# Kernel tuning notes

Measured on AMD Instinct MI355X. Metric: run time of the kernel, lower is better.

The kernel has to match this reference:

```python
import jax, jax.numpy as jnp
import numpy as np

FREQ_DIM = 64
BLOCK_DIM = 64
N = 256          # lattice sites
CH = 6           # channel_num -> block diagonals at offsets -1, 0, +1
S = 2 * 16 + CH - 2   # seq_num = 36
BS = 4           # block_size (kron of two 2x2 matrices)
HID = 128
EPS = 1e-5
B = 32

_e = np.eye(2)
_sx = np.array([[0., 1.], [1., 0.]])
_siy = np.array([[0., 1.], [-1., 0.]])
_sz = np.array([[1., 0.], [0., -1.]])
_p = [_e, _sx, _siy, _sz]
KRONS = jnp.asarray(np.stack([np.kron(_p[a], _p[b]) for a in range(4) for b in range(4)]).astype(np.float32))  # (16,4,4)
Z1 = KRONS[12]  # kron(sigma_z, I) used for interaction blocks ('z1')


def _bn(h, g, b):
    # BatchNorm1d in training mode: biased batch statistics over axis 0
    mu = h.mean(axis=0)
    v = h.var(axis=0)
    return g * (h - mu) / jnp.sqrt(v + EPS) + b


def _mlp(x, Win, bin_, Wmid, bmid, Wout, bout, gamma, beta):
    # depth-4 MLP: Lin+ReLU, then (BN,Lin,ReLU) x2, then BN,Lin,ReLU
    h = jax.nn.relu(x @ Win + bin_)
    for i in range(Wmid.shape[0]):
        h = jax.nn.relu(_bn(h, gamma[i], beta[i]) @ Wmid[i] + bmid[i])
    return jax.nn.relu(_bn(h, gamma[-1], beta[-1]) @ Wout + bout)


def _lstm(xs, h0, c0, Wih, Whh, bih, bhh):
    # xs: (B, T, S); torch gate order i, f, g, o
    def step(carry, x_t):
        h, c = carry
        gates = x_t @ Wih.T + h @ Whh.T + (bih + bhh)
        i, f, g, o = jnp.split(gates, 4, axis=-1)
        c = jax.nn.sigmoid(f) * c + jax.nn.sigmoid(i) * jnp.tanh(g)
        h = jax.nn.sigmoid(o) * jnp.tanh(c)
        return (h, c), h
    _, hs = jax.lax.scan(step, (h0, c0), jnp.swapaxes(xs, 0, 1))
    return jnp.swapaxes(hs, 0, 1)


def setup_inputs() -> dict:
    key = jax.random.key(0)
    ks = iter(jax.random.split(key, 48))
    def w(shape, s=0.05):
        return jax.random.normal(next(ks), shape, dtype=jnp.float32) * s
    d = {
        'x': w((B, FREQ_DIM + BLOCK_DIM), 1.0),
        'fd_Win': w((FREQ_DIM, HID)), 'fd_bin': w((HID,)),
        'fd_Wmid': w((2, HID, HID)), 'fd_bmid': w((2, HID)),
        'fd_Wout': w((HID, S)), 'fd_bout': w((S,)),
        'fd_gamma': jnp.ones((3, HID), jnp.float32), 'fd_beta': jnp.zeros((3, HID), jnp.float32),
        'bd_Win': w((BLOCK_DIM, HID)), 'bd_bin': w((HID,)),
        'bd_Wmid': w((2, HID, HID)), 'bd_bmid': w((2, HID)),
        'bd_Wout': w((HID, S)), 'bd_bout': w((S,)),
        'bd_gamma': jnp.ones((3, HID), jnp.float32), 'bd_beta': jnp.zeros((3, HID), jnp.float32),
        'sc_Win': w((S, 1, HID)), 'sc_bin': w((S, HID)),
        'sc_Wmid': w((S, 2, HID, HID)), 'sc_bmid': w((S, 2, HID)),
        'sc_Wout': w((S, HID, N)), 'sc_bout': w((S, N)),
        'sc_gamma': jnp.ones((S, 3, HID), jnp.float32), 'sc_beta': jnp.zeros((S, 3, HID), jnp.float32),
        'lstm_Wih': w((4 * S, S)), 'lstm_Whh': w((4 * S, S)),
        'lstm_bih': w((4 * S,)), 'lstm_bhh': w((4 * S,)),
        'mix_W': w((S, 2 * S)), 'mix_b': w((S,)),
    }
    return d


def reference(x, fd_Win, fd_bin, fd_Wmid, fd_bmid, fd_Wout, fd_bout, fd_gamma, fd_beta,
              bd_Win, bd_bin, bd_Wmid, bd_bmid, bd_Wout, bd_bout, bd_gamma, bd_beta,
              sc_Win, sc_bin, sc_Wmid, sc_bmid, sc_Wout, sc_bout, sc_gamma, sc_beta,
              lstm_Wih, lstm_Whh, lstm_bih, lstm_bhh, mix_W, mix_b):
    Bsz = x.shape[0]
    block = _mlp(x[:, FREQ_DIM:], bd_Win, bd_bin, bd_Wmid, bd_bmid, bd_Wout, bd_bout, bd_gamma, bd_beta)  # (B,S)
    freq = _mlp(x[:, :FREQ_DIM], fd_Win, fd_bin, fd_Wmid, fd_bmid, fd_Wout, fd_bout, fd_gamma, fd_beta)   # (B,S)
    # S independent scalar->N MLPs, batched with vmap over the stacked params
    sc = jax.vmap(_mlp)(freq.T[:, :, None], sc_Win, sc_bin, sc_Wmid, sc_bmid,
                        sc_Wout, sc_bout, sc_gamma, sc_beta)  # (S,B,N)
    freq_seq = jnp.cos(sc).transpose(1, 2, 0)   # (B,N,S)
    seq = _lstm(freq_seq, block, jnp.zeros_like(block), lstm_Wih, lstm_Whh, lstm_bih, lstm_bhh)  # (B,N,S)
    block_seq = jnp.concatenate([jnp.broadcast_to(block[:, :, None], (Bsz, S, N)),
                                 jnp.swapaxes(seq, 1, 2)], axis=1)  # (B,2S,N)
    # 1x1 Conv2d == channel mixing matmul
    mixed = jnp.einsum('bcn,oc->bon', block_seq, mix_W) + mix_b[None, :, None]  # (B,S,N)
    inter = mixed[:, :CH - 2]                          # (B,CH-2,N)
    onsite = mixed[:, CH - 2:].reshape(Bsz, 2, 16, N)  # (B,2,16,N)
    H_int = jnp.einsum('bcn,ij->bcnij', inter, Z1)         # (B,CH-2,N,4,4)
    H_os = jnp.einsum('bgkn,kij->bgnij', onsite, KRONS)    # (B,2,N,4,4) summed over 16 pairs
    half = (CH - 2) // 2
    strips = jnp.concatenate([H_int[:, :half], H_os, H_int[:, half:]], axis=1)  # (B,CH,N,4,4)
    strips = strips.reshape(Bsz, CH // 2, 2, N, BS, BS)
    # banded block assembly: strip i lives on block-diagonal offset i - (CH//2)//2
    grid = jnp.zeros((Bsz, 2, N, N, BS, BS), dtype=x.dtype)
    for i in range(CH // 2):
        o = i - (CH // 2) // 2
        rows = jnp.arange(N - abs(o)) + max(0, -o)
        cols = rows + o
        grid = grid.at[:, :, rows, cols].set(strips[:, i][:, :, rows])
    matrix = grid.transpose(0, 1, 2, 4, 3, 5).reshape(Bsz, 2, N * BS, N * BS)
    return matrix
```

## Files before the change

### kernel.cpp

```cpp
#include <hip/hip_runtime.h>
#include <math.h>

#define EPSF 1e-5f
typedef __attribute__((ext_vector_type(2))) float f32x2;
typedef __attribute__((ext_vector_type(4))) float f32x4;

__device__ __forceinline__ float pauliv(int p, int r, int c) {
    switch (p) {
        case 0: return (r == c) ? 1.f : 0.f;
        case 1: return (r != c) ? 1.f : 0.f;
        case 2: return (r == 0 && c == 1) ? 1.f : ((r == 1 && c == 0) ? -1.f : 0.f);
        default: return (r == c) ? ((r == 0) ? 1.f : -1.f) : 0.f;
    }
}

__device__ void mlp64_body(const float* __restrict__ xin,
                           const float* __restrict__ Win,
                           const float* __restrict__ bin_,
                           const float* __restrict__ Wmid,
                           const float* __restrict__ bmid,
                           const float* __restrict__ Wout,
                           const float* __restrict__ bout,
                           const float* __restrict__ gamma,
                           const float* __restrict__ beta,
                           float* __restrict__ out)
{
    __shared__ float sX[2048];
    __shared__ float sA[4096];
    __shared__ float sB[4096];
    __shared__ float sMu[128], sRs[128];
    int tid = threadIdx.x;

    for (int idx = tid; idx < 2048; idx += 1024) {
        int b = idx >> 6, c = idx & 63;
        sX[idx] = xin[b * 128 + c];
    }
    __syncthreads();

    for (int idx = tid; idx < 4096; idx += 1024) {
        int b = idx >> 7, j = idx & 127;
        float acc = bin_[j];
        for (int c = 0; c < 64; ++c) acc = fmaf(sX[b * 64 + c], Win[c * 128 + j], acc);
        sA[idx] = fmaxf(acc, 0.f);
    }
    __syncthreads();

    float* cur = sA;
    float* nxt = sB;
    for (int l = 0; l < 3; ++l) {
        if (tid < 128) {
            float s = 0.f, s2 = 0.f;
            for (int b = 0; b < 32; ++b) {
                float v = cur[b * 128 + tid];
                s += v; s2 += v * v;
            }
            float mu = s * (1.f / 32.f);
            float var = s2 * (1.f / 32.f) - mu * mu;
            sMu[tid] = mu;
            sRs[tid] = rsqrtf(var + EPSF);
        }
        __syncthreads();
        for (int idx = tid; idx < 4096; idx += 1024) {
            int j = idx & 127;
            cur[idx] = gamma[l * 128 + j] * (cur[idx] - sMu[j]) * sRs[j] + beta[l * 128 + j];
        }
        __syncthreads();
        if (l < 2) {
            for (int idx = tid; idx < 4096; idx += 1024) {
                int b = idx >> 7, j = idx & 127;
                float acc = bmid[l * 128 + j];
                for (int c = 0; c < 128; ++c)
                    acc = fmaf(cur[b * 128 + c], Wmid[(l * 128 + c) * 128 + j], acc);
                nxt[idx] = fmaxf(acc, 0.f);
            }
            __syncthreads();
            float* t = cur; cur = nxt; nxt = t;
        } else {
            for (int idx = tid; idx < 1152; idx += 1024) {
                int b = idx / 36, j = idx - b * 36;
                float acc = bout[j];
                for (int c = 0; c < 128; ++c)
                    acc = fmaf(cur[b * 128 + c], Wout[c * 36 + j], acc);
                out[idx] = fmaxf(acc, 0.f);
            }
        }
    }
}

__global__ __launch_bounds__(1024) void k_mlp2(
    const float* __restrict__ x,
    const float* fdWin, const float* fdbin, const float* fdWmid, const float* fdbmid,
    const float* fdWout, const float* fdbout, const float* fdg, const float* fdbt,
    const float* bdWin, const float* bdbin, const float* bdWmid, const float* bdbmid,
    const float* bdWout, const float* bdbout, const float* bdg, const float* bdbt,
    float* freq, float* blk)
{
    if (blockIdx.x == 0)
        mlp64_body(x + 64, bdWin, bdbin, bdWmid, bdbmid, bdWout, bdbout, bdg, bdbt, blk);
    else
        mlp64_body(x, fdWin, fdbin, fdWmid, fdbmid, fdWout, fdbout, fdg, fdbt, freq);
}

__global__ __launch_bounds__(512) void k_sc1(
    const float* __restrict__ freq,
    const float* __restrict__ Win,
    const float* __restrict__ bin_,
    const float* __restrict__ Wmid,
    const float* __restrict__ bmid,
    const float* __restrict__ gamma,
    const float* __restrict__ beta,
    float* __restrict__ actW)
{
    int s = blockIdx.x, tid = threadIdx.x;
    __shared__ float sA[4096];
    __shared__ float sB[4096];
    __shared__ float sMu[128], sRs[128];
    const float* Wm = Wmid + (size_t)s * 2 * 128 * 128;
    const float* gm = gamma + s * 3 * 128;
    const float* bt = beta + s * 3 * 128;

    for (int idx = tid; idx < 4096; idx += 512) {
        int b = idx >> 7, j = idx & 127;
        float acc = fmaf(freq[b * 36 + s], Win[s * 128 + j], bin_[s * 128 + j]);
        sA[idx] = fmaxf(acc, 0.f);
    }
    __syncthreads();

    float* cur = sA;
    float* nxt = sB;
    for (int l = 0; l < 3; ++l) {
        if (tid < 128) {
            float sm = 0.f, s2 = 0.f;
            for (int b = 0; b < 32; ++b) {
                float v = cur[b * 128 + tid];
                sm += v; s2 += v * v;
            }
            float mu = sm * (1.f / 32.f);
            float var = s2 * (1.f / 32.f) - mu * mu;
            sMu[tid] = mu;
            sRs[tid] = rsqrtf(var + EPSF);
        }
        __syncthreads();
        for (int idx = tid; idx < 4096; idx += 512) {
            int j = idx & 127;
            cur[idx] = gm[l * 128 + j] * (cur[idx] - sMu[j]) * sRs[j] + bt[l * 128 + j];
        }
        __syncthreads();
        if (l < 2) {
            int jj = tid & 127, bb = tid >> 7;
            float acc[8];
            #pragma unroll
            for (int k = 0; k < 8; ++k) acc[k] = bmid[(s * 2 + l) * 128 + jj];
            for (int c = 0; c < 128; ++c) {
                float w = Wm[(l * 128 + c) * 128 + jj];
                #pragma unroll
                for (int k = 0; k < 8; ++k)
                    acc[k] = fmaf(cur[(bb + 4 * k) * 128 + c], w, acc[k]);
            }
            __syncthreads();
            #pragma unroll
            for (int k = 0; k < 8; ++k) nxt[(bb + 4 * k) * 128 + jj] = fmaxf(acc[k], 0.f);
            __syncthreads();
            float* t = cur; cur = nxt; nxt = t;
        } else {
            for (int idx = tid; idx < 4096; idx += 512)
                actW[(size_t)s * 4096 + idx] = cur[idx];
        }
    }
}

__global__ __launch_bounds__(512) void k_sc2(
    const float* __restrict__ actW,
    const float* __restrict__ Wout,
    const float* __restrict__ bout,
    float* __restrict__ fseq2)
{
    int bidx = blockIdx.x;
    int s = bidx >> 2, q = bidx & 3;
    int tid = threadIdx.x;
    __shared__ float sAct[4096];
    for (int idx = tid; idx < 4096; idx += 512)
        sAct[idx] = actW[(size_t)s * 4096 + idx];
    __syncthreads();

    int nn = (tid & 63) + q * 64;
    int bb = tid >> 6;
    const float* Wo = Wout + (size_t)s * 128 * 256;
    float acc[4];
    #pragma unroll
    for (int k = 0; k < 4; ++k) acc[k] = bout[s * 256 + nn];
    #pragma unroll 4
    for (int c = 0; c < 128; ++c) {
        float w = Wo[c * 256 + nn];
        #pragma unroll
        for (int k = 0; k < 4; ++k)
            acc[k] = fmaf(sAct[(bb + 8 * k) * 128 + c], w, acc[k]);
    }
    #pragma unroll
    for (int k = 0; k < 4; ++k) {
        float v = fmaxf(acc[k], 0.f);
        fseq2[((size_t)s * 32 + bb + 8 * k) * 256 + nn] = __cosf(v);
    }
}

__global__ __launch_bounds__(512) void k_xg(
    const float* __restrict__ fseq2, const float* __restrict__ Wih,
    const float* __restrict__ bih, const float* __restrict__ bhh,
    float* __restrict__ Xg)
{
    int t = blockIdx.x, tid = threadIdx.x;
    __shared__ float sF[1152];
    __shared__ float sWt[36 * 144];
    for (int idx = tid; idx < 1152; idx += 512) {
        int s = idx >> 5, b = idx & 31;
        sF[b * 36 + s] = fseq2[(size_t)idx * 256 + t];
    }
    for (int idx = tid; idx < 5184; idx += 512) {
        int j = idx / 36, s = idx - j * 36;
        sWt[s * 144 + j] = Wih[idx];
    }
    __syncthreads();
    for (int idx = tid; idx < 4608; idx += 512) {
        int b = idx / 144, j = idx - b * 144;
        int g = j / 36, u = j - g * 36;
        float acc = bih[j] + bhh[j];
        #pragma unroll
        for (int s = 0; s < 36; ++s)
            acc = fmaf(sF[b * 36 + s], sWt[s * 144 + j], acc);
        Xg[(((size_t)b * 256 + t) * 36 + u) * 4 + g] = acc;
    }
}

#define PF 8
__global__ __launch_bounds__(64, 1) void k_lstm(
    const float* __restrict__ Xg,
    const float* __restrict__ blk,
    const float* __restrict__ Whh,
    float* __restrict__ hseq2)
{
    int b = blockIdx.x;
    int lane = threadIdx.x;
    int uu = lane < 36 ? lane : 35;
    bool active = lane < 36;

    f32x2 wif[36], wgo[36];
    #pragma unroll
    for (int k = 0; k < 36; ++k) {
        wif[k] = f32x2{Whh[uu * 36 + k], Whh[(36 + uu) * 36 + k]};
        wgo[k] = f32x2{Whh[(72 + uu) * 36 + k], Whh[(108 + uu) * 36 + k]};
    }
    float h = blk[b * 36 + uu];
    float c = 0.f;
    const f32x4* xb = (const f32x4*)(Xg + (size_t)b * 256 * 144);
    float* hout = hseq2 + (size_t)b * 256 * 36;

    f32x4 pipe[PF];
    #pragma unroll
    for (int i = 0; i < PF; ++i) pipe[i] = xb[i * 36 + uu];

    #pragma unroll 8
    for (int t = 0; t < 256; ++t) {
        f32x4 xg4 = pipe[t & (PF - 1)];
        if (t + PF < 256) pipe[t & (PF - 1)] = xb[(t + PF) * 36 + uu];

        f32x2 a0 = f32x2{xg4.x, xg4.y};
        f32x2 b0 = f32x2{xg4.z, xg4.w};
        f32x2 a1 = f32x2{0.f, 0.f};
        f32x2 b1 = f32x2{0.f, 0.f};
        #pragma unroll
        for (int k = 0; k < 36; k += 2) {
            float h0 = __int_as_float(__builtin_amdgcn_readlane(__float_as_int(h), k));
            float h1 = __int_as_float(__builtin_amdgcn_readlane(__float_as_int(h), k + 1));
            a0 = __builtin_elementwise_fma(wif[k], f32x2{h0, h0}, a0);
            b0 = __builtin_elementwise_fma(wgo[k], f32x2{h0, h0}, b0);
            a1 = __builtin_elementwise_fma(wif[k + 1], f32x2{h1, h1}, a1);
            b1 = __builtin_elementwise_fma(wgo[k + 1], f32x2{h1, h1}, b1);
        }
        a0 += a1; b0 += b1;
        float iv = 1.f / (1.f + __expf(-a0.x));
        float fv = 1.f / (1.f + __expf(-a0.y));
        float gv = 1.f - 2.f / (__expf(2.f * b0.x) + 1.f);
        float ov = 1.f / (1.f + __expf(-b0.y));
        c = fmaf(fv, c, iv * gv);
        h = ov * (1.f - 2.f / (__expf(2.f * c) + 1.f));
        if (active) hout[t * 36 + uu] = h;
    }
}

__global__ __launch_bounds__(256) void k_mixed(
    const float* __restrict__ blk, const float* __restrict__ hseq2,
    const float* __restrict__ mixW, const float* __restrict__ mixb,
    float* __restrict__ mixed)
{
    int bq = blockIdx.x;
    int b = bq >> 2, oq = bq & 3;
    int tid = threadIdx.x;
    __shared__ float sH[256 * 37];
    __shared__ float sW[9 * 36];
    __shared__ float sBase[9];
    for (int idx = tid; idx < 9216; idx += 256) {
        int t = idx / 36, u = idx - t * 36;
        sH[t * 37 + u] = hseq2[(size_t)b * 9216 + idx];
    }
    for (int idx = tid; idx < 9 * 36; idx += 256) {
        int o = idx / 36, u = idx - o * 36;
        sW[idx] = mixW[(oq * 9 + o) * 72 + 36 + u];
    }
    if (tid < 9) {
        int o = oq * 9 + tid;
        float acc = mixb[o];
        for (int c = 0; c < 36; ++c) acc = fmaf(mixW[o * 72 + c], blk[b * 36 + c], acc);
        sBase[tid] = acc;
    }
    __syncthreads();
    int n = tid;
    #pragma unroll
    for (int o = 0; o < 9; ++o) {
        float acc = sBase[o];
        #pragma unroll
        for (int u = 0; u < 36; ++u)
            acc = fmaf(sW[o * 36 + u], sH[n * 37 + u], acc);
        mixed[((size_t)b * 36 + oq * 9 + o) * 256 + n] = acc;
    }
}

__global__ __launch_bounds__(256) void k_out(
    const float* __restrict__ mixed, float* __restrict__ out)
{
    int bid = blockIdx.x;
    int bg = bid >> 5, chunk = bid & 31;
    int g = bg & 1, b = bg >> 1;
    float* base = out + (size_t)bg * (1024 * 1024);
    f32x4* rp = (f32x4*)(base + (size_t)chunk * 32 * 1024);
    f32x4 z = f32x4{0.f, 0.f, 0.f, 0.f};
    #pragma unroll
    for (int i = 0; i < 32; ++i)
        rp[i * 256 + threadIdx.x] = z;
    __syncthreads();

    int tid = threadIdx.x;
    if (tid < 8) {
        int n = chunk * 8 + tid;
        const float* mb = mixed + (size_t)b * 36 * 256;
        float vSub = mb[(size_t)g * 256 + n];
        float vSup = mb[(size_t)(2 + g) * 256 + n];
        float ch[16];
        #pragma unroll
        for (int k = 0; k < 16; ++k) ch[k] = mb[(size_t)(4 + 16 * g + k) * 256 + n];
        float d[16];
        #pragma unroll
        for (int e = 0; e < 16; ++e) {
            int r = e >> 2, cc = e & 3;
            float acc = 0.f;
            #pragma unroll
            for (int k = 0; k < 16; ++k) {
                float kv = pauliv(k >> 2, r >> 1, cc >> 1) * pauliv(k & 3, r & 1, cc & 1);
                if (kv == 1.f) acc = acc + ch[k];
                else if (kv == -1.f) acc = acc - ch[k];
            }
            d[e] = acc;
        }
        #pragma unroll
        for (int r = 0; r < 4; ++r)
            *(f32x4*)(base + (size_t)(4 * n + r) * 1024 + 4 * n) =
                f32x4{d[r * 4 + 0], d[r * 4 + 1], d[r * 4 + 2], d[r * 4 + 3]};
        if (n > 0) {
            #pragma unroll
            for (int r = 0; r < 4; ++r)
                base[(size_t)(4 * n + r) * 1024 + 4 * (n - 1) + r] = (r < 2) ? vSub : -vSub;
        }
        if (n < 255) {
            #pragma unroll
            for (int r = 0; r < 4; ++r)
                base[(size_t)(4 * n + r) * 1024 + 4 * (n + 1) + r] = (r < 2) ? vSup : -vSup;
        }
    }
}

extern "C" void kernel_launch(void* const* d_in, const int* in_sizes, int n_in,
                              void* d_out, int out_size, void* d_ws, size_t ws_size,
                              hipStream_t stream) {
    const float* x      = (const float*)d_in[0];
    const float* fdWin  = (const float*)d_in[1];
    const float* fdbin  = (const float*)d_in[2];
    const float* fdWmid = (const float*)d_in[3];
    const float* fdbmid = (const float*)d_in[4];
    const float* fdWout = (const float*)d_in[5];
    const float* fdbout = (const float*)d_in[6];
    const float* fdg    = (const float*)d_in[7];
    const float* fdbt   = (const float*)d_in[8];
    const float* bdWin  = (const float*)d_in[9];
    const float* bdbin  = (const float*)d_in[10];
    const float* bdWmid = (const float*)d_in[11];
    const float* bdbmid = (const float*)d_in[12];
    const float* bdWout = (const float*)d_in[13];
    const float* bdbout = (const float*)d_in[14];
    const float* bdg    = (const float*)d_in[15];
    const float* bdbt   = (const float*)d_in[16];
    const float* scWin  = (const float*)d_in[17];
    const float* scbin  = (const float*)d_in[18];
    const float* scWmid = (const float*)d_in[19];
    const float* scbmid = (const float*)d_in[20];
    const float* scWout = (const float*)d_in[21];
    const float* scbout = (const float*)d_in[22];
    const float* scg    = (const float*)d_in[23];
    const float* scbt   = (const float*)d_in[24];
    const float* Wih    = (const float*)d_in[25];
    const float* Whh    = (const float*)d_in[26];
    const float* bih    = (const float*)d_in[27];
    const float* bhh    = (const float*)d_in[28];
    const float* mixW   = (const float*)d_in[29];
    const float* mixb   = (const float*)d_in[30];

    float* ws    = (float*)d_ws;
    float* freq  = ws;
    float* blk   = ws + 1152;
    float* fseq2 = ws + 2304;
    float* Xg    = ws + 297216;
    float* hseq2 = ws + 1476864;
    float* mixed = ws + 1771776;
    float* actW  = Xg;

    float* out = (float*)d_out;

    k_mlp2<<<2, 1024, 0, stream>>>(x,
        fdWin, fdbin, fdWmid, fdbmid, fdWout, fdbout, fdg, fdbt,
        bdWin, bdbin, bdWmid, bdbmid, bdWout, bdbout, bdg, bdbt,
        freq, blk);
    k_sc1<<<36, 512, 0, stream>>>(freq, scWin, scbin, scWmid, scbmid, scg, scbt, actW);
    k_sc2<<<144, 512, 0, stream>>>(actW, scWout, scbout, fseq2);
    k_xg<<<256, 512, 0, stream>>>(fseq2, Wih, bih, bhh, Xg);
    k_lstm<<<32, 64, 0, stream>>>(Xg, blk, Whh, hseq2);
    k_mixed<<<128, 256, 0, stream>>>(blk, hseq2, mixW, mixb, mixed);
    k_out<<<2048, 256, 0, stream>>>(mixed, out);
}
```

Baseline: 350.9 us.

## Split LSTM gate computation across two wavefronts with LDS exchange

The LSTM recurrence kernel now runs two wavefronts per batch element. Each computes two of the four gates, so the per-lane matvec work and register footprint are halved. The g/o gate activations are passed through shared memory to wave 0, which updates the cell and hidden state and broadcasts h back through LDS. This trades serial FMA latency per timestep for two block-wide barriers per step on the critical recurrence path.

```diff
diff --git a/kernel.cpp b/kernel.cpp
--- a/kernel.cpp
+++ b/kernel.cpp
@@ -4,6 +4,9 @@
 #define EPSF 1e-5f
 typedef __attribute__((ext_vector_type(2))) float f32x2;
 typedef __attribute__((ext_vector_type(4))) float f32x4;
+
+__device__ __forceinline__ float sigf(float x) { return 1.f / (1.f + __expf(-x)); }
+__device__ __forceinline__ float tanhf_fast(float x) { return 1.f - 2.f / (__expf(2.f * x) + 1.f); }
 
 __device__ __forceinline__ float pauliv(int p, int r, int c) {
     switch (p) {
@@ -232,58 +235,71 @@
 }
 
 #define PF 8
-__global__ __launch_bounds__(64, 1) void k_lstm(
+__global__ __launch_bounds__(128) void k_lstm(
     const float* __restrict__ Xg,
     const float* __restrict__ blk,
     const float* __restrict__ Whh,
     float* __restrict__ hseq2)
 {
+    __shared__ f32x2 sGO[40];
+    __shared__ float sH[40];
+
     int b = blockIdx.x;
-    int lane = threadIdx.x;
+    int wid = threadIdx.x >> 6;
+    int lane = threadIdx.x & 63;
     int uu = lane < 36 ? lane : 35;
     bool active = lane < 36;
 
-    f32x2 wif[36], wgo[36];
+    f32x2 w2[36];
+    {
+        const float* wA = Whh + (size_t)(wid * 72 + uu) * 36;
+        const float* wB = Whh + (size_t)(wid * 72 + 36 + uu) * 36;
+        #pragma unroll
+        for (int k = 0; k < 36; ++k) w2[k] = f32x2{wA[k], wB[k]};
+    }
+
+    float hv = blk[b * 36 + uu];
+    float c = 0.f;
+    const f32x2* xb2 = (const f32x2*)(Xg + (size_t)b * 256 * 144);
+    float* hout = hseq2 + (size_t)b * 256 * 36;
+
+    f32x2 pipe[PF];
     #pragma unroll
-    for (int k = 0; k < 36; ++k) {
-        wif[k] = f32x2{Whh[uu * 36 + k], Whh[(36 + uu) * 36 + k]};
-        wgo[k] = f32x2{Whh[(72 + uu) * 36 + k], Whh[(108 + uu) * 36 + k]};
-    }
-    float h = blk[b * 36 + uu];
-    float c = 0.f;
-    const f32x4* xb = (const f32x4*)(Xg + (size_t)b * 256 * 144);
-    float* hout = hseq2 + (size_t)b * 256 * 36;
-
-    f32x4 pipe[PF];
-    #pragma unroll
-    for (int i = 0; i < PF; ++i) pipe[i] = xb[i * 36 + uu];
+    for (int i = 0; i < PF; ++i) pipe[i] = xb2[(i * 36 + uu) * 2 + wid];
 
     #pragma unroll 8
     for (int t = 0; t < 256; ++t) {
-        f32x4 xg4 = pipe[t & (PF - 1)];
-        if (t + PF < 256) pipe[t & (PF - 1)] = xb[(t + PF) * 36 + uu];
-
-        f32x2 a0 = f32x2{xg4.x, xg4.y};
-        f32x2 b0 = f32x2{xg4.z, xg4.w};
+        f32x2 a0 = pipe[t & (PF - 1)];
+        if (t + PF < 256) pipe[t & (PF - 1)] = xb2[((t + PF) * 36 + uu) * 2 + wid];
+
         f32x2 a1 = f32x2{0.f, 0.f};
-        f32x2 b1 = f32x2{0.f, 0.f};
         #pragma unroll
         for (int k = 0; k < 36; k += 2) {
-            float h0 = __int_as_float(__builtin_amdgcn_readlane(__float_as_int(h), k));
-            float h1 = __int_as_float(__builtin_amdgcn_readlane(__float_as_int(h), k + 1));
-            a0 = __builtin_elementwise_fma(wif[k], f32x2{h0, h0}, a0);
-            b0 = __builtin_elementwise_fma(wgo[k], f32x2{h0, h0}, b0);
-            a1 = __builtin_elementwise_fma(wif[k + 1], f32x2{h1, h1}, a1);
-            b1 = __builtin_elementwise_fma(wgo[k + 1], f32x2{h1, h1}, b1);
-        }
-        a0 += a1; b0 += b1;
-        float iv = 1.f / (1.f + __expf(-a0.x));
-        float fv = 1.f / (1.f + __expf(-a0.y));
-        float gv = 1.f - 2.f / (__expf(2.f * b0.x) + 1.f);
-        float ov = 1.f / (1.f + __expf(-b0.y));
-        c = fmaf(fv, c, iv * gv);
-        h = ov * (1.f - 2.f / (__expf(2.f * c) + 1.f));
-        if (active) hout[t * 36 + uu] = h;
+            float h0 = __int_as_float(__builtin_amdgcn_readlane(__float_as_int(hv), k));
+            float h1 = __int_as_float(__builtin_amdgcn_readlane(__float_as_int(hv), k + 1));
+            a0 = __builtin_elementwise_fma(w2[k], f32x2{h0, h0}, a0);
+            a1 = __builtin_elementwise_fma(w2[k + 1], f32x2{h1, h1}, a1);
+        }
+        a0 += a1;
+
+        if (wid == 1 && active) {
+            float gv = tanhf_fast(a0.x);
+            float ov = sigf(a0.y);
+            sGO[uu] = f32x2{gv, ov};
+        }
+        __syncthreads();
+        if (wid == 0 && active) {
+            float iv = sigf(a0.x);
+            float fv = sigf(a0.y);
+            f32x2 go = sGO[uu];
+            c = fmaf(fv, c, iv * go.x);
+            float hn = go.y * tanhf_fast(c);
+            hv = hn;
+            sH[uu] = hn;
+            hout[t * 36 + uu] = hn;
+        }
+        __syncthreads();
+        if (wid == 1) hv = sH[uu];
     }
 }
 
@@ -430,7 +446,7 @@
     k_sc1<<<36, 512, 0, stream>>>(freq, scWin, scbin, scWmid, scbmid, scg, scbt, actW);
     k_sc2<<<144, 512, 0, stream>>>(actW, scWout, scbout, fseq2);
     k_xg<<<256, 512, 0, stream>>>(fseq2, Wih, bih, bhh, Xg);
-    k_lstm<<<32, 64, 0, stream>>>(Xg, blk, Whh, hseq2);
+    k_lstm<<<32, 128, 0, stream>>>(Xg, blk, Whh, hseq2);
     k_mixed<<<128, 256, 0, stream>>>(blk, hseq2, mixW, mixb, mixed);
     k_out<<<2048, 256, 0, stream>>>(mixed, out);
 }
```

Result: no change. 356.8 us (+1.7%).
